# Kernel tuning notes

Hardware: AMD Instinct MI355X
Metric: run time of the kernel (lower is better)

Reference implementation:

```python
import jax, jax.numpy as jnp
import numpy as np

B, C, H, W = 16, 512, 64, 64
WS = 16            # window size -> N = 256 tokens per window
NH = 16            # num heads, head_dim = 32
HD = C // NH
HID = int((4 * C * 0.5) / 64) * 64   # SwiGLU hidden = 1024
CPB = 512
EPS = 1e-5


def _rel_tables(ws):
    r = np.arange(-(ws - 1), ws, dtype=np.float32)
    tab = np.stack(np.meshgrid(r, r, indexing='ij'), axis=-1)  # (2ws-1,2ws-1,2)
    tab = tab / (ws - 1)
    tab = tab * 8.0
    tab = np.sign(tab) * np.log2(np.abs(tab) + 1.0) / np.log2(8.0)
    # relative position index (N,N)
    coords = np.stack(np.meshgrid(np.arange(ws), np.arange(ws), indexing='ij'))
    cf = coords.reshape(2, -1)
    rel = (cf[:, :, None] - cf[:, None, :]).transpose(1, 2, 0).astype(np.int64)
    rel[:, :, 0] += ws - 1
    rel[:, :, 1] += ws - 1
    rel[:, :, 0] *= 2 * ws - 1
    idx = rel.sum(-1)
    return tab.reshape(-1, 2), idx


def setup_inputs() -> dict:
    key = jax.random.key(0)
    ks = jax.random.split(key, 12)
    s = 0.02
    tab, idx = _rel_tables(WS)
    return {
        'x': jax.random.normal(ks[0], (B, C, H, W), jnp.float32),
        'rel_table': jnp.asarray(tab),
        'norm1_w': jnp.ones((C,), jnp.float32),
        'norm1_b': jnp.zeros((C,), jnp.float32),
        'norm2_w': jnp.ones((C,), jnp.float32),
        'norm2_b': jnp.zeros((C,), jnp.float32),
        'qkv_w': jax.random.normal(ks[1], (C, 3 * C), jnp.float32) * s,
        'proj_w': jax.random.normal(ks[2], (C, C), jnp.float32) * s,
        'cpb_w1': jax.random.normal(ks[3], (2, CPB), jnp.float32) * s,
        'cpb_b1': jnp.zeros((CPB,), jnp.float32),
        'cpb_w2': jax.random.normal(ks[4], (CPB, NH), jnp.float32) * s,
        'fc1_w': jax.random.normal(ks[5], (C, 2 * HID), jnp.float32) * s,
        'fc2_w': jax.random.normal(ks[6], (HID, C), jnp.float32) * s,
        'rel_index': jnp.asarray(idx),
    }


def _ln(x, w, b):
    m = jnp.mean(x, axis=-1, keepdims=True)
    v = jnp.mean(jnp.square(x - m), axis=-1, keepdims=True)
    return (x - m) * jax.lax.rsqrt(v + EPS) * w + b


def reference(x, rel_table, norm1_w, norm1_b, norm2_w, norm2_b, qkv_w, proj_w,
              cpb_w1, cpb_b1, cpb_w2, fc1_w, fc2_w, rel_index):
    ws, nh, hd = WS, NH, HD
    N = ws * ws
    # window partition: (B,C,H,W) -> (B*nW, N, C)
    xw = x.reshape(B, C, H // ws, ws, W // ws, ws)
    xw = xw.transpose(0, 2, 4, 3, 5, 1).reshape(-1, N, C)
    Bw = xw.shape[0]

    # --- window attention ---
    h = _ln(xw, norm1_w, norm1_b)
    qkv = (h @ qkv_w).reshape(Bw, N, 3, nh, hd).transpose(2, 0, 3, 1, 4)
    q, k, v = qkv[0], qkv[1], qkv[2]          # (Bw, nh, N, hd)
    attn = jnp.einsum('bhnd,bhmd->bhnm', q, k) * (hd ** -0.5)
    # Swin-v2 continuous position bias MLP + gather
    bias_tab = jax.nn.relu(rel_table @ cpb_w1 + cpb_b1) @ cpb_w2   # ((2ws-1)^2, nh)
    bias = bias_tab[rel_index]                 # (N, N, nh)
    bias = 16.0 * jax.nn.sigmoid(bias.transpose(2, 0, 1))          # (nh, N, N)
    attn = jax.nn.softmax(attn + bias[None], axis=-1)
    o = jnp.einsum('bhnm,bhmd->bhnd', attn, v)
    o = o.transpose(0, 2, 1, 3).reshape(Bw, N, C) @ proj_w
    xw = xw + o

    # --- SwiGLU MLP ---
    h2 = _ln(xw, norm2_w, norm2_b)
    u = h2 @ fc1_w
    val, gate = jnp.split(u, 2, axis=-1)       # Mlp/SwiGLU: chunk -> silu(gate)*x
    xw = xw + (jax.nn.silu(gate) * val) @ fc2_w

    # window reverse + outer skip
    xr = xw.reshape(B, H // ws, W // ws, ws, ws, C)
    xr = xr.transpose(0, 5, 1, 3, 2, 4).reshape(B, C, H, W)
    return xr + x
```

## Files before the change

kernel.cpp:

```cpp
#include <hip/hip_runtime.h>
#include <hip/hip_bf16.h>

typedef unsigned short u16;
typedef unsigned int u32;
typedef __attribute__((ext_vector_type(8))) u16 u16x8;
typedef __attribute__((ext_vector_type(4))) u16 u16x4;
typedef __attribute__((ext_vector_type(8))) short bf16x8;
typedef __attribute__((ext_vector_type(4))) float f32x4;

__device__ __forceinline__ u16 f2bf(float f) {
  u32 u = __float_as_uint(f);
  u += 0x7fffu + ((u >> 16) & 1u);
  return (u16)(u >> 16);
}
__device__ __forceinline__ float bf2f(u16 h) {
  return __uint_as_float(((u32)h) << 16);
}
__device__ __forceinline__ u16 cvt_bf(float f) {
  __hip_bfloat16 h(f);
  return __builtin_bit_cast(u16, h);
}
__device__ __forceinline__ bf16x8 ld_bf8(const u16* p) {
  return __builtin_bit_cast(bf16x8, *(const u16x8*)p);
}

#if __has_builtin(__builtin_amdgcn_exp2f)
#define EXP2(x) __builtin_amdgcn_exp2f(x)
#else
#define EXP2(x) exp2f(x)
#endif

typedef const void __attribute__((address_space(1)))* gas_t;
typedef void __attribute__((address_space(3)))* las_t;
#define GLOAD_LDS16(gp, lp) __builtin_amdgcn_global_load_lds((gas_t)(gp), (las_t)(lp), 16, 0, 0)

#define QSCALE 0.25503486f
#define BIAS_MUL 23.08312065f

__global__ __launch_bounds__(256, 4) void head_kernel(
    const float* __restrict__ x, const float* __restrict__ n1w, const float* __restrict__ n1b,
    u16* __restrict__ hbuf, u16* __restrict__ xwbuf,
    const float* __restrict__ qkv_w, const float* __restrict__ proj_w,
    const float* __restrict__ fc1_w, const float* __restrict__ fc2_w,
    const float* __restrict__ rt, const float* __restrict__ cw1,
    const float* __restrict__ cb1, const float* __restrict__ cw2,
    u16* __restrict__ wq, u16* __restrict__ wp, u16* __restrict__ w1,
    u16* __restrict__ w2, float* __restrict__ tab2) {
  __shared__ u16 tile[512 * 33];
  __shared__ float red[2][8][32];
  __shared__ float meanv[32], rstdv[32];
  int blk = blockIdx.x, t = threadIdx.x;
  if (blk < 2048) {
    int bi = blk;
    int bimg = bi >> 7, rest = bi & 127, hrow = rest >> 1, half = rest & 1;
    int p = t & 31, g = t >> 5;
    const float* xr = x + (size_t)bimg * 512 * 4096 + (size_t)hrow * 64 + half * 32;
    float s = 0.f, s2 = 0.f;
    for (int i = 0; i < 64; ++i) {
      int c = g * 64 + i;
      float v = xr[(size_t)c * 4096 + p];
      tile[c * 33 + p] = f2bf(v);
      s += v; s2 += v * v;
    }
    red[0][g][p] = s; red[1][g][p] = s2;
    __syncthreads();
    if (t < 32) {
      float ss = 0.f, qq = 0.f;
      for (int gg = 0; gg < 8; ++gg) { ss += red[0][gg][t]; qq += red[1][gg][t]; }
      float mu = ss * (1.f / 512.f);
      float var = qq * (1.f / 512.f) - mu * mu;
      meanv[t] = mu;
      rstdv[t] = rsqrtf(var + 1e-5f);
    }
    __syncthreads();
    int c0 = t * 2;
    float w0 = n1w[c0], w1v = n1w[c0 + 1], b0 = n1b[c0], b1v = n1b[c0 + 1];
    int hy = hrow >> 4, iy = hrow & 15;
    for (int pp = 0; pp < 32; ++pp) {
      int pixel = half * 32 + pp;
      int wx = pixel >> 4, ix = pixel & 15;
      int widx = bimg * 16 + hy * 4 + wx;
      size_t basep = ((size_t)widx * 256 + iy * 16 + ix) * 512;
      u16 rb0 = tile[c0 * 33 + pp], rb1 = tile[(c0 + 1) * 33 + pp];
      float mu = meanv[pp], rs = rstdv[pp];
      float v0 = bf2f(rb0), v1 = bf2f(rb1);
      *(u32*)(xwbuf + basep + c0) = (u32)rb0 | ((u32)rb1 << 16);
      u16 h0 = f2bf((v0 - mu) * rs * w0 + b0);
      u16 h1 = f2bf((v1 - mu) * rs * w1v + b1v);
      *(u32*)(hbuf + basep + c0) = (u32)h0 | ((u32)h1 << 16);
    }
    return;
  }
  int b = blk - 2048;
  if (b < 3072) {
    int idx = b * 256 + t;
    int n = idx >> 9, k = idx & 511;
    float s = n < 512 ? QSCALE : 1.f;
    wq[idx] = f2bf(qkv_w[(size_t)k * 1536 + n] * s);
  } else if (b < 4096) {
    int idx = (b - 3072) * 256 + t;
    int n = idx >> 9, k = idx & 511;
    wp[idx] = f2bf(proj_w[(size_t)k * 512 + n]);
  } else if (b < 8192) {
    int idx = (b - 4096) * 256 + t;
    int n = idx >> 9, k = idx & 511;
    int i = ((n >> 5) << 4) | (n & 15);
    int gsel = (n >> 4) & 1;
    w1[idx] = f2bf(fc1_w[(size_t)k * 2048 + i + gsel * 1024]);
  } else if (b < 10240) {
    int idx = (b - 8192) * 256 + t;
    int n = idx >> 10, k = idx & 1023;
    w2[idx] = f2bf(fc2_w[(size_t)k * 512 + n]);
  } else {
    float* hid = (float*)tile;
    float (*part)[17] = (float (*)[17])(tile + 4096);
    int tix = b - 10240;
    float r0 = rt[tix * 2], r1 = rt[tix * 2 + 1];
    for (int j = t; j < 512; j += 256) {
      float v = r0 * cw1[j] + r1 * cw1[512 + j] + cb1[j];
      hid[j] = v > 0.f ? v : 0.f;
    }
    __syncthreads();
    int hh = t & 15, seg = t >> 4;
    float acc = 0.f;
    for (int j = seg * 32; j < seg * 32 + 32; ++j) acc += hid[j] * cw2[j * 16 + hh];
    part[seg][hh] = acc;
    __syncthreads();
    if (t < 16) {
      float s = 0.f;
      for (int g = 0; g < 16; ++g) s += part[g][t];
      tab2[t * 961 + tix] = BIAS_MUL / (1.f + __expf(-s)) - 23.0f;
    }
  }
}

template <int EPI>
__global__ __launch_bounds__(256, 4) void gemm_bt(
    const u16* __restrict__ A, const u16* __restrict__ Bt,
    u16* __restrict__ out, const u16* __restrict__ res,
    const float* __restrict__ xg, float* __restrict__ outf,
    int M, int N, int K) {
  __shared__ u16 As[128 * 64];
  __shared__ u16 Bs[128 * 64];
  const int t = threadIdx.x, l = t & 63, wv = t >> 6;
  const int nbx = N >> 7;
  const int wg = (int)blockIdx.x;
  const int xcd = wg & 7, c = wg >> 3;
  const int cm = c / nbx;
  const int m0 = (xcd * 64 + cm) * 128, n0 = (c - cm * nbx) * 128;
  const int wr = wv >> 1, wc = wv & 1;
  const int lr = l & 15, lk = l >> 4;
  f32x4 acc[4][4] = {};
  for (int kt = 0; kt < K; kt += 64) {
#pragma unroll
    for (int j = 0; j < 4; ++j) {
      int qi = j * 256 + t;
      int r = qi >> 3, c8 = (qi & 7) * 8;
      GLOAD_LDS16(A + (size_t)(m0 + r) * K + kt + c8, As + (size_t)(j * 256 + wv * 64) * 8);
    }
#pragma unroll
    for (int j = 0; j < 4; ++j) {
      int qi = j * 256 + t;
      int r = qi >> 3, c8 = (qi & 7) * 8;
      GLOAD_LDS16(Bt + (size_t)(n0 + r) * K + kt + c8, Bs + (size_t)(j * 256 + wv * 64) * 8);
    }
    __syncthreads();
#pragma unroll
    for (int ks = 0; ks < 2; ++ks) {
      bf16x8 a[4], bb[4];
#pragma unroll
      for (int mf = 0; mf < 4; ++mf)
        a[mf] = ld_bf8(As + (wr * 64 + mf * 16 + lr) * 64 + ks * 32 + lk * 8);
#pragma unroll
      for (int nf = 0; nf < 4; ++nf)
        bb[nf] = ld_bf8(Bs + (wc * 64 + nf * 16 + lr) * 64 + ks * 32 + lk * 8);
#pragma unroll
      for (int mf = 0; mf < 4; ++mf)
#pragma unroll
        for (int nf = 0; nf < 4; ++nf)
          acc[mf][nf] = __builtin_amdgcn_mfma_f32_16x16x32_bf16(a[mf], bb[nf], acc[mf][nf], 0, 0, 0);
    }
    __syncthreads();
  }
#pragma unroll
  for (int mf = 0; mf < 4; ++mf) {
    int rbase = m0 + wr * 64 + mf * 16 + lk * 4;
    if constexpr (EPI == 3) {
#pragma unroll
      for (int nf = 0; nf < 4; nf += 2) {
        int colv = n0 + wc * 64 + nf * 16 + lr;
        int i = ((colv >> 5) << 4) | (colv & 15);
#pragma unroll
        for (int jj = 0; jj < 4; ++jj) {
          int row = rbase + jj;
          float val = acc[mf][nf][jj], gate = acc[mf][nf + 1][jj];
          float sil = gate / (1.f + __expf(-gate));
          out[(size_t)row * 1024 + i] = f2bf(sil * val);
        }
      }
    } else if constexpr (EPI == 4) {
      int widx = rbase >> 8, iy = (rbase >> 4) & 15, ix0 = rbase & 15;
      int bimg = widx >> 4, hy = (widx >> 2) & 3, wx = widx & 3;
#pragma unroll
      for (int nf = 0; nf < 4; ++nf) {
        int col = n0 + wc * 64 + nf * 16 + lr;
        size_t obase = (((size_t)(bimg * 512 + col) * 64) + hy * 16 + iy) * 64 + wx * 16 + ix0;
        const float* xp = xg + obase;
        float* op = outf + obase;
#pragma unroll
        for (int jj = 0; jj < 4; ++jj)
          op[jj] = acc[mf][nf][jj] + bf2f(res[(size_t)(rbase + jj) * 512 + col]) + xp[jj];
      }
    } else if constexpr (EPI == 1) {
#pragma unroll
      for (int nf = 0; nf < 4; ++nf) {
        int col = n0 + wc * 64 + nf * 16 + lr;
#pragma unroll
        for (int jj = 0; jj < 4; ++jj) {
          int row = rbase + jj;
          out[(size_t)row * N + col] = f2bf(acc[mf][nf][jj] + bf2f(res[(size_t)row * N + col]));
        }
      }
    } else {
#pragma unroll
      for (int nf = 0; nf < 4; ++nf) {
        int col = n0 + wc * 64 + nf * 16 + lr;
#pragma unroll
        for (int jj = 0; jj < 4; ++jj)
          out[(size_t)(rbase + jj) * N + col] = f2bf(acc[mf][nf][jj]);
      }
    }
  }
}

__global__ __launch_bounds__(256, 4) void attn_kernel(
    const u16* __restrict__ qkv, const float* __restrict__ tab2, u16* __restrict__ ob) {
  __shared__ u16 vt[32 * 72];
  __shared__ float tabh4[31 * 32 * 4];
  __shared__ u16 pl[4][16 * 76];
  const int h = blockIdx.x, w = blockIdx.y;
  const int t = threadIdx.x, l = t & 63, wid = t >> 6;
  const u16* qg = qkv + (size_t)(w * 256) * 1536 + h * 32;
  const u16* kg = qg + 512;
  const u16* vg = qg + 1024;
  const float* th = tab2 + h * 961;
  for (int i = t; i < 992; i += 256) {
    int dy = i >> 5, dx = i & 31;
#pragma unroll
    for (int r = 0; r < 4; ++r) {
      int dxr = dx + r;
      tabh4[i * 4 + r] = (dxr <= 30) ? th[dy * 31 + dxr] : 0.f;
    }
  }
  const int q4 = l >> 4, c0 = l & 15;
  const int dx0 = q4 * 4 - c0 + 15;
  bf16x8 qa[4];
#pragma unroll
  for (int mf = 0; mf < 4; ++mf)
    qa[mf] = ld_bf8(qg + (size_t)(wid * 64 + mf * 16 + c0) * 1536 + q4 * 8);
  f32x4 oacc[4][2] = {};
  float psum[4][4] = {};
  for (int ct = 0; ct < 4; ++ct) {
    {
      int r = t & 63, j = t >> 6;
      u16x8 dv = *(const u16x8*)(vg + (size_t)(ct * 64 + r) * 1536 + j * 8);
#pragma unroll
      for (int e = 0; e < 8; ++e) vt[(j * 8 + e) * 72 + r] = dv[e];
    }
    __syncthreads();
    bf16x8 bfr[4];
#pragma unroll
    for (int nf = 0; nf < 4; ++nf)
      bfr[nf] = ld_bf8(kg + (size_t)(ct * 64 + nf * 16 + c0) * 1536 + q4 * 8);
    bf16x8 vfr[2][2];
#pragma unroll
    for (int df = 0; df < 2; ++df)
#pragma unroll
      for (int ks2 = 0; ks2 < 2; ++ks2)
        vfr[df][ks2] = ld_bf8(vt + (df * 16 + c0) * 72 + ks2 * 32 + q4 * 8);
#pragma unroll
    for (int mf = 0; mf < 4; ++mf) {
      const int dyb = wid * 4 + mf - ct * 4 + 15;
      f32x4 sacc[4];
#pragma unroll
      for (int nf = 0; nf < 4; ++nf)
        sacc[nf] = *(const f32x4*)&tabh4[((dyb - nf) * 32 + dx0) * 4];
      __builtin_amdgcn_s_setprio(1);
#pragma unroll
      for (int nf = 0; nf < 4; ++nf)
        sacc[nf] = __builtin_amdgcn_mfma_f32_16x16x32_bf16(qa[mf], bfr[nf], sacc[nf], 0, 0, 0);
      __builtin_amdgcn_s_setprio(0);
#pragma unroll
      for (int nf = 0; nf < 4; ++nf) {
#pragma unroll
        for (int jj = 0; jj < 4; ++jj) {
          float p = EXP2(sacc[nf][jj]);
          psum[mf][jj] += p;
          pl[wid][(q4 * 4 + jj) * 76 + nf * 16 + c0] = cvt_bf(p);
        }
      }
      __builtin_amdgcn_s_setprio(1);
#pragma unroll
      for (int ks2 = 0; ks2 < 2; ++ks2) {
        bf16x8 pa = ld_bf8(&pl[wid][c0 * 76 + ks2 * 32 + q4 * 8]);
        oacc[mf][0] = __builtin_amdgcn_mfma_f32_16x16x32_bf16(pa, vfr[0][ks2], oacc[mf][0], 0, 0, 0);
        oacc[mf][1] = __builtin_amdgcn_mfma_f32_16x16x32_bf16(pa, vfr[1][ks2], oacc[mf][1], 0, 0, 0);
      }
      __builtin_amdgcn_s_setprio(0);
    }
    __syncthreads();
  }
#pragma unroll
  for (int mf = 0; mf < 4; ++mf) {
#pragma unroll
    for (int jj = 0; jj < 4; ++jj) {
      float s = psum[mf][jj];
      s += __shfl_xor(s, 1);
      s += __shfl_xor(s, 2);
      s += __shfl_xor(s, 4);
      s += __shfl_xor(s, 8);
      float inv = 1.f / s;
      int row = wid * 64 + mf * 16 + q4 * 4 + jj;
      size_t obase = ((size_t)w * 256 + row) * 512 + h * 32;
      ob[obase + c0] = f2bf(oacc[mf][0][jj] * inv);
      ob[obase + 16 + c0] = f2bf(oacc[mf][1][jj] * inv);
    }
  }
}

__global__ __launch_bounds__(256, 4) void ln2_kernel(const u16* __restrict__ r1,
    const float* __restrict__ w, const float* __restrict__ b, u16* __restrict__ h2) {
  int t = threadIdx.x, l = t & 63, wid = t >> 6;
  size_t token = (size_t)blockIdx.x * 4 + wid;
  const u16* rp = r1 + token * 512 + l * 8;
  u16x8 raw = *(const u16x8*)rp;
  float v[8]; float s = 0.f, s2 = 0.f;
#pragma unroll
  for (int i = 0; i < 8; ++i) { v[i] = bf2f(raw[i]); s += v[i]; s2 += v[i] * v[i]; }
#pragma unroll
  for (int m = 1; m < 64; m <<= 1) { s += __shfl_xor(s, m); s2 += __shfl_xor(s2, m); }
  float mu = s * (1.f / 512.f);
  float var = s2 * (1.f / 512.f) - mu * mu;
  float rs = rsqrtf(var + 1e-5f);
  u16x8 o;
#pragma unroll
  for (int i = 0; i < 8; ++i) {
    int c = l * 8 + i;
    o[i] = f2bf((v[i] - mu) * rs * w[c] + b[c]);
  }
  *(u16x8*)(h2 + token * 512 + l * 8) = o;
}

extern "C" void kernel_launch(void* const* d_in, const int* in_sizes, int n_in,
                              void* d_out, int out_size, void* d_ws, size_t ws_size,
                              hipStream_t stream) {
  (void)in_sizes; (void)n_in; (void)out_size; (void)ws_size;
  const float* x = (const float*)d_in[0];
  const float* rel_table = (const float*)d_in[1];
  const float* n1w = (const float*)d_in[2];
  const float* n1b = (const float*)d_in[3];
  const float* n2w = (const float*)d_in[4];
  const float* n2b = (const float*)d_in[5];
  const float* qkv_w = (const float*)d_in[6];
  const float* proj_w = (const float*)d_in[7];
  const float* cpb_w1 = (const float*)d_in[8];
  const float* cpb_b1 = (const float*)d_in[9];
  const float* cpb_w2 = (const float*)d_in[10];
  const float* fc1_w = (const float*)d_in[11];
  const float* fc2_w = (const float*)d_in[12];
  float* outp = (float*)d_out;
  char* ws = (char*)d_ws;

  u16* wq = (u16*)(ws + 0);
  u16* wp = (u16*)(ws + 1572864);
  u16* w1 = (u16*)(ws + 2097152);
  u16* w2 = (u16*)(ws + 4194304);
  float* tab2 = (float*)(ws + 5242880);
  const size_t RB = 67108864;
  u16* R0 = (u16*)(ws + 8388608);
  u16* R1 = (u16*)(ws + 8388608 + RB);
  u16* R2 = (u16*)(ws + 8388608 + 2 * RB);
  u16* R3 = (u16*)(ws + 8388608 + 3 * RB);
  u16* R4 = (u16*)(ws + 8388608 + 4 * RB);

  head_kernel<<<13249, 256, 0, stream>>>(x, n1w, n1b, R2, R0,
                                         qkv_w, proj_w, fc1_w, fc2_w,
                                         rel_table, cpb_w1, cpb_b1, cpb_w2,
                                         wq, wp, w1, w2, tab2);
  gemm_bt<0><<<6144, 256, 0, stream>>>(R2, wq, R3, nullptr,
                                       nullptr, nullptr, 65536, 1536, 512);
  attn_kernel<<<dim3(16, 256), 256, 0, stream>>>(R3, tab2, R2);
  gemm_bt<1><<<2048, 256, 0, stream>>>(R2, wp, R1, R0,
                                       nullptr, nullptr, 65536, 512, 512);
  ln2_kernel<<<16384, 256, 0, stream>>>(R1, n2w, n2b, R3);
  gemm_bt<3><<<8192, 256, 0, stream>>>(R3, w1, R4, nullptr,
                                       nullptr, nullptr, 65536, 2048, 512);
  gemm_bt<4><<<2048, 256, 0, stream>>>(R4, w2, nullptr, R1,
                                       x, outp, 65536, 512, 1024);
}
```

Before: 746.0 us.

## XOR-swizzle GEMM LDS tiles and precompute expanded bias table in global memory

The GEMM now permutes 16-byte chunks within each 64-element row of the LDS tiles, XORing the chunk index with the row index, and applies the same swizzle on the MFMA operand reads. This is meant to remove LDS bank conflicts on the row-strided fragment loads. Separately, the head kernel writes the 4-way shifted bias table directly in the layout attention uses, after a memset zeroes the padding. Each attention block then copies it with vector loads instead of gathering and rebuilding it. The cost is one extra memset and a larger bias table in global memory.

New measurement: 721.7 us. -3.2%, faster.

```diff
diff --git a/kernel.cpp b/kernel.cpp
--- a/kernel.cpp
+++ b/kernel.cpp
@@ -45,7 +45,7 @@
     const float* __restrict__ rt, const float* __restrict__ cw1,
     const float* __restrict__ cb1, const float* __restrict__ cw2,
     u16* __restrict__ wq, u16* __restrict__ wp, u16* __restrict__ w1,
-    u16* __restrict__ w2, float* __restrict__ tab2) {
+    u16* __restrict__ w2, float* __restrict__ tabh4g) {
   __shared__ u16 tile[512 * 33];
   __shared__ float red[2][8][32];
   __shared__ float meanv[32], rstdv[32];
@@ -129,7 +129,14 @@
     if (t < 16) {
       float s = 0.f;
       for (int g = 0; g < 16; ++g) s += part[g][t];
-      tab2[t * 961 + tix] = BIAS_MUL / (1.f + __expf(-s)) - 23.0f;
+      float val = BIAS_MUL / (1.f + __expf(-s)) - 23.0f;
+      int dy = tix / 31, c = tix - dy * 31;
+#pragma unroll
+      for (int r = 0; r < 4; ++r) {
+        int dx = c - r;
+        if (dx >= 0)
+          tabh4g[((size_t)t * 992 + dy * 32 + dx) * 4 + r] = val;
+      }
     }
   }
 }
@@ -150,19 +157,22 @@
   const int m0 = (xcd * 64 + cm) * 128, n0 = (c - cm * nbx) * 128;
   const int wr = wv >> 1, wc = wv & 1;
   const int lr = l & 15, lk = l >> 4;
+  const int swz = lr & 7;
   f32x4 acc[4][4] = {};
   for (int kt = 0; kt < K; kt += 64) {
 #pragma unroll
     for (int j = 0; j < 4; ++j) {
       int qi = j * 256 + t;
-      int r = qi >> 3, c8 = (qi & 7) * 8;
-      GLOAD_LDS16(A + (size_t)(m0 + r) * K + kt + c8, As + (size_t)(j * 256 + wv * 64) * 8);
+      int r = qi >> 3, s = qi & 7;
+      int c8 = (s ^ (r & 7)) * 8;
+      GLOAD_LDS16(A + (size_t)(m0 + r) * K + kt + c8, As + (size_t)qi * 8);
     }
 #pragma unroll
     for (int j = 0; j < 4; ++j) {
       int qi = j * 256 + t;
-      int r = qi >> 3, c8 = (qi & 7) * 8;
-      GLOAD_LDS16(Bt + (size_t)(n0 + r) * K + kt + c8, Bs + (size_t)(j * 256 + wv * 64) * 8);
+      int r = qi >> 3, s = qi & 7;
+      int c8 = (s ^ (r & 7)) * 8;
+      GLOAD_LDS16(Bt + (size_t)(n0 + r) * K + kt + c8, Bs + (size_t)qi * 8);
     }
     __syncthreads();
 #pragma unroll
@@ -170,10 +180,10 @@
       bf16x8 a[4], bb[4];
 #pragma unroll
       for (int mf = 0; mf < 4; ++mf)
-        a[mf] = ld_bf8(As + (wr * 64 + mf * 16 + lr) * 64 + ks * 32 + lk * 8);
+        a[mf] = ld_bf8(As + (wr * 64 + mf * 16 + lr) * 64 + (((ks * 4 + lk) ^ swz) << 3));
 #pragma unroll
       for (int nf = 0; nf < 4; ++nf)
-        bb[nf] = ld_bf8(Bs + (wc * 64 + nf * 16 + lr) * 64 + ks * 32 + lk * 8);
+        bb[nf] = ld_bf8(Bs + (wc * 64 + nf * 16 + lr) * 64 + (((ks * 4 + lk) ^ swz) << 3));
 #pragma unroll
       for (int mf = 0; mf < 4; ++mf)
 #pragma unroll
@@ -234,7 +244,7 @@
 }
 
 __global__ __launch_bounds__(256, 4) void attn_kernel(
-    const u16* __restrict__ qkv, const float* __restrict__ tab2, u16* __restrict__ ob) {
+    const u16* __restrict__ qkv, const float* __restrict__ tabh4g, u16* __restrict__ ob) {
   __shared__ u16 vt[32 * 72];
   __shared__ float tabh4[31 * 32 * 4];
   __shared__ u16 pl[4][16 * 76];
@@ -243,15 +253,9 @@
   const u16* qg = qkv + (size_t)(w * 256) * 1536 + h * 32;
   const u16* kg = qg + 512;
   const u16* vg = qg + 1024;
-  const float* th = tab2 + h * 961;
-  for (int i = t; i < 992; i += 256) {
-    int dy = i >> 5, dx = i & 31;
-#pragma unroll
-    for (int r = 0; r < 4; ++r) {
-      int dxr = dx + r;
-      tabh4[i * 4 + r] = (dxr <= 30) ? th[dy * 31 + dxr] : 0.f;
-    }
-  }
+  const float* tg = tabh4g + (size_t)h * 992 * 4;
+  for (int i = t; i < 992; i += 256)
+    *(f32x4*)&tabh4[i * 4] = *(const f32x4*)(tg + (size_t)i * 4);
   const int q4 = l >> 4, c0 = l & 15;
   const int dx0 = q4 * 4 - c0 + 15;
   bf16x8 qa[4];
@@ -375,7 +379,7 @@
   u16* wp = (u16*)(ws + 1572864);
   u16* w1 = (u16*)(ws + 2097152);
   u16* w2 = (u16*)(ws + 4194304);
-  float* tab2 = (float*)(ws + 5242880);
+  float* tabh4g = (float*)(ws + 5242880);
   const size_t RB = 67108864;
   u16* R0 = (u16*)(ws + 8388608);
   u16* R1 = (u16*)(ws + 8388608 + RB);
@@ -383,13 +387,14 @@
   u16* R3 = (u16*)(ws + 8388608 + 3 * RB);
   u16* R4 = (u16*)(ws + 8388608 + 4 * RB);
 
+  hipMemsetAsync(tabh4g, 0, (size_t)16 * 992 * 4 * sizeof(float), stream);
   head_kernel<<<13249, 256, 0, stream>>>(x, n1w, n1b, R2, R0,
                                          qkv_w, proj_w, fc1_w, fc2_w,
                                          rel_table, cpb_w1, cpb_b1, cpb_w2,
-                                         wq, wp, w1, w2, tab2);
+                                         wq, wp, w1, w2, tabh4g);
   gemm_bt<0><<<6144, 256, 0, stream>>>(R2, wq, R3, nullptr,
                                        nullptr, nullptr, 65536, 1536, 512);
-  attn_kernel<<<dim3(16, 256), 256, 0, stream>>>(R3, tab2, R2);
+  attn_kernel<<<dim3(16, 256), 256, 0, stream>>>(R3, tabh4g, R2);
   gemm_bt<1><<<2048, 256, 0, stream>>>(R2, wp, R1, R0,
                                        nullptr, nullptr, 65536, 512, 512);
   ln2_kernel<<<16384, 256, 0, stream>>>(R1, n2w, n2b, R3);
```
